# Performance work log

Measured on AMD Instinct MI355X. Metric: run time of the kernel, lower is better.

Reference implementation:

```python
import jax, jax.numpy as jnp
import numpy as np

IN_CH = 4096
OUT_CH = 4096
DENSITY = 0.1
BATCH = 8192


def setup_inputs() -> dict:
    key = jax.random.key(0)
    k_mask, k_w, k_b, k_x = jax.random.split(key, 4)
    # Fixed sparsity pattern, as in the torch module's sparse_mask.nonzero()
    mask = jax.random.bernoulli(k_mask, DENSITY, (OUT_CH, IN_CH))
    rows, cols = jnp.nonzero(mask)  # unique (row, col) pairs
    rows = rows.astype(jnp.int32)
    cols = cols.astype(jnp.int32)
    nnz = rows.shape[0]
    # Kaiming-style init per output row (approximate: uniform bound from mean fan-in)
    fan_in = jnp.maximum(jnp.sum(mask, axis=1).astype(jnp.float32), 1.0)  # [OUT_CH]
    gain = np.sqrt(2.0 / (1.0 + 5.0))  # leaky_relu gain with a=sqrt(5)
    std = gain / jnp.sqrt(fan_in)
    w_bound = np.sqrt(3.0) * std  # per-row bound
    u = jax.random.uniform(k_w, (nnz,), minval=-1.0, maxval=1.0)
    sparse_weight = u * w_bound[rows]
    b_bound = 1.0 / jnp.sqrt(fan_in)
    bias = jax.random.uniform(k_b, (OUT_CH,), minval=-1.0, maxval=1.0) * b_bound
    x = jax.random.normal(k_x, (BATCH, IN_CH), dtype=jnp.float32)
    return {
        "x": x,
        "sparse_weight": sparse_weight.astype(jnp.float32),
        "rows": rows,
        "cols": cols,
        "bias": bias.astype(jnp.float32),
    }


def reference(x, sparse_weight, rows, cols, bias):
    # Rebuild the (fixed-pattern) sparse weight as a dense [OUT_CH, IN_CH] matrix
    # (indices are unique, so .set matches the COO semantics), then y = x @ W^T + b.
    W = jnp.zeros((OUT_CH, IN_CH), dtype=sparse_weight.dtype).at[rows, cols].set(sparse_weight)
    return x @ W.T + bias  # [BATCH, OUT_CH]
```

## Files before the change

kernel.cpp:

```cpp
#include <hip/hip_runtime.h>
#include <hip/hip_bf16.h>

#define M_DIM 8192
#define N_DIM 4096
#define K_DIM 4096
#define BM 128
#define BN 128
#define BK 64

typedef __bf16 bf16x8 __attribute__((ext_vector_type(8)));
typedef float  f32x4  __attribute__((ext_vector_type(4)));
typedef unsigned short u16x8 __attribute__((ext_vector_type(8)));

#define ASYNC16(g, l)                                                          \
  __builtin_amdgcn_global_load_lds(                                            \
      (__attribute__((address_space(1))) void*)(g),                            \
      (__attribute__((address_space(3))) void*)(l), 16, 0, 0)

static __device__ __forceinline__ unsigned short f2bf(float f) {
  unsigned int u = __float_as_uint(f);
  u += 0x7fffu + ((u >> 16) & 1u);
  return (unsigned short)(u >> 16);
}

__global__ void sl_bounds(const int* __restrict__ rows, int* __restrict__ row_start,
                          int* __restrict__ row_end, int nnz) {
  int k = blockIdx.x * 256 + threadIdx.x;
  if (k >= nnz) return;
  int r = rows[k];
  if (k == 0 || rows[k - 1] != r) row_start[r] = k;
  if (k == nnz - 1 || rows[k + 1] != r) row_end[r] = k + 1;
}

__global__ __launch_bounds__(256) void sl_prep(
    const float4* __restrict__ x4, u16x8* __restrict__ xb,
    const float* __restrict__ vals, const int* __restrict__ cols,
    const int* __restrict__ row_start, const int* __restrict__ row_end,
    unsigned short* __restrict__ W) {
  const int b = blockIdx.x;
  if (b < N_DIM) {
    __shared__ __align__(16) unsigned short rowbuf[K_DIM];
    u16x8* rb8 = (u16x8*)rowbuf;
    u16x8 z = {};
    rb8[threadIdx.x] = z;
    rb8[256 + threadIdx.x] = z;
    __syncthreads();
    const int s = row_start[b];
    const int e = row_end[b];
    for (int k = s + threadIdx.x; k < e; k += 256)
      rowbuf[cols[k]] = f2bf(vals[k]);
    __syncthreads();
    u16x8* dst = (u16x8*)(W + (size_t)b * K_DIM);
    dst[threadIdx.x] = rb8[threadIdx.x];
    dst[256 + threadIdx.x] = rb8[256 + threadIdx.x];
  } else {
    const int i = (b - N_DIM) * 256 + threadIdx.x;
    float4 a = x4[2 * i];
    float4 c = x4[2 * i + 1];
    u16x8 o;
    o[0] = f2bf(a.x); o[1] = f2bf(a.y); o[2] = f2bf(a.z); o[3] = f2bf(a.w);
    o[4] = f2bf(c.x); o[5] = f2bf(c.y); o[6] = f2bf(c.z); o[7] = f2bf(c.w);
    xb[i] = o;
  }
}

__global__ __launch_bounds__(256) void sl_prep_bs(
    const float4* __restrict__ x4, u16x8* __restrict__ xb,
    const float* __restrict__ vals, const int* __restrict__ rows,
    const int* __restrict__ cols, unsigned short* __restrict__ W, int nnz) {
  const int b = blockIdx.x;
  if (b < N_DIM) {
    __shared__ __align__(16) unsigned short rowbuf[K_DIM];
    u16x8* rb8 = (u16x8*)rowbuf;
    u16x8 z = {};
    rb8[threadIdx.x] = z;
    rb8[256 + threadIdx.x] = z;
    __syncthreads();
    int l = 0, h = nnz;
    while (l < h) { int m = (l + h) >> 1; if (rows[m] < b) l = m + 1; else h = m; }
    const int s = l;
    h = nnz;
    while (l < h) { int m = (l + h) >> 1; if (rows[m] <= b) l = m + 1; else h = m; }
    const int e = l;
    for (int k = s + threadIdx.x; k < e; k += 256)
      rowbuf[cols[k]] = f2bf(vals[k]);
    __syncthreads();
    u16x8* dst = (u16x8*)(W + (size_t)b * K_DIM);
    dst[threadIdx.x] = rb8[threadIdx.x];
    dst[256 + threadIdx.x] = rb8[256 + threadIdx.x];
  } else {
    const int i = (b - N_DIM) * 256 + threadIdx.x;
    float4 a = x4[2 * i];
    float4 c = x4[2 * i + 1];
    u16x8 o;
    o[0] = f2bf(a.x); o[1] = f2bf(a.y); o[2] = f2bf(a.z); o[3] = f2bf(a.w);
    o[4] = f2bf(c.x); o[5] = f2bf(c.y); o[6] = f2bf(c.z); o[7] = f2bf(c.w);
    xb[i] = o;
  }
}

__global__ __launch_bounds__(256, 3) void sl_gemm_bias(
    const unsigned short* __restrict__ A,
    const unsigned short* __restrict__ B,
    const float* __restrict__ bias,
    float* __restrict__ C) {
  __shared__ __align__(16) unsigned short As[BM * BK];
  __shared__ __align__(16) unsigned short Bs[BN * BK];

  const int tid  = threadIdx.x;
  const int wave = tid >> 6;
  const int lane = tid & 63;
  const int m0 = blockIdx.x * BM;
  const int n0 = blockIdx.y * BN;

  const int srow = tid >> 3;
  const int scol = ((tid & 7) ^ ((tid >> 3) & 7)) * 8;
  const unsigned short* gA = A + (size_t)(m0 + srow) * K_DIM + scol;
  const unsigned short* gB = B + (size_t)(n0 + srow) * K_DIM + scol;
  unsigned short* lA = As + (size_t)(wave * 64) * 8;
  unsigned short* lB = Bs + (size_t)(wave * 64) * 8;
  const size_t GROW = (size_t)32 * K_DIM;
  const size_t LROW = (size_t)256 * 8;

  const int wm   = (wave >> 1) * 64;
  const int wn   = (wave & 1) * 64;
  const int fm   = lane & 15;
  const int quad = lane >> 4;
  const int sw   = fm & 7;

  f32x4 acc[4][4] = {};

#pragma unroll
  for (int r = 0; r < 4; ++r) {
    ASYNC16(gA + r * GROW, lA + r * LROW);
    ASYNC16(gB + r * GROW, lB + r * LROW);
  }
  gA += BK; gB += BK;

  for (int k0 = 0; k0 < K_DIM; k0 += BK) {
    __syncthreads();

    bf16x8 af[4][2], bfr[4][2];
#pragma unroll
    for (int t = 0; t < 4; ++t) {
#pragma unroll
      for (int h = 0; h < 2; ++h) {
        const int pA = ((h * 4 + quad) ^ sw) * 8;
        af[t][h]  = *(const bf16x8*)(As + (size_t)(wm + t * 16 + fm) * BK + pA);
        bfr[t][h] = *(const bf16x8*)(Bs + (size_t)(wn + t * 16 + fm) * BK + pA);
      }
    }
    __syncthreads();

    if (k0 + BK < K_DIM) {
#pragma unroll
      for (int r = 0; r < 4; ++r) {
        ASYNC16(gA + r * GROW, lA + r * LROW);
        ASYNC16(gB + r * GROW, lB + r * LROW);
      }
      gA += BK; gB += BK;
    }

#pragma unroll
    for (int h = 0; h < 2; ++h)
#pragma unroll
      for (int tm = 0; tm < 4; ++tm)
#pragma unroll
        for (int tn = 0; tn < 4; ++tn)
          acc[tm][tn] = __builtin_amdgcn_mfma_f32_16x16x32_bf16(
              af[tm][h], bfr[tn][h], acc[tm][tn], 0, 0, 0);
  }

  float bv[4];
#pragma unroll
  for (int tn = 0; tn < 4; ++tn) bv[tn] = bias[n0 + wn + tn * 16 + fm];

#pragma unroll
  for (int tm = 0; tm < 4; ++tm) {
    const int mbase = m0 + wm + tm * 16 + quad * 4;
#pragma unroll
    for (int tn = 0; tn < 4; ++tn) {
      const int n = n0 + wn + tn * 16 + fm;
      float* p = C + (size_t)mbase * N_DIM + n;
#pragma unroll
      for (int r = 0; r < 4; ++r)
        __builtin_nontemporal_store(acc[tm][tn][r] + bv[tn], p + (size_t)r * N_DIM);
    }
  }
}

__global__ void sl_naive(const float* __restrict__ x, const float* __restrict__ vals,
                         const int* __restrict__ rows, const int* __restrict__ cols,
                         const float* __restrict__ bias, float* __restrict__ out,
                         int nnz) {
  const int o = blockIdx.x;
  int l = 0, h = nnz;
  while (l < h) { int m = (l + h) >> 1; if (rows[m] < o) l = m + 1; else h = m; }
  const int s = l;
  h = nnz;
  while (l < h) { int m = (l + h) >> 1; if (rows[m] <= o) l = m + 1; else h = m; }
  const int e = l;
  const float bv = bias[o];
  for (int b = threadIdx.x; b < M_DIM; b += blockDim.x) {
    float acc = bv;
    const float* xb = x + (size_t)b * K_DIM;
    for (int k = s; k < e; ++k) acc += vals[k] * xb[cols[k]];
    out[(size_t)b * N_DIM + o] = acc;
  }
}

extern "C" void kernel_launch(void* const* d_in, const int* in_sizes, int n_in,
                              void* d_out, int out_size, void* d_ws, size_t ws_size,
                              hipStream_t stream) {
  const float* x    = (const float*)d_in[0];
  const float* vals = (const float*)d_in[1];
  const int*   rows = (const int*)d_in[2];
  const int*   cols = (const int*)d_in[3];
  const float* bias = (const float*)d_in[4];
  float* out = (float*)d_out;
  const int nnz = in_sizes[1];

  const size_t xb_bytes  = (size_t)M_DIM * K_DIM * 2;
  const size_t w_bytes   = (size_t)N_DIM * K_DIM * 2;
  const size_t idx_bytes = (size_t)2 * N_DIM * 4;

  const int cvt_blocks = (M_DIM * K_DIM) / 8 / 256;

  if (ws_size >= xb_bytes + w_bytes + idx_bytes) {
    unsigned short* xb = (unsigned short*)d_ws;
    unsigned short* W  = (unsigned short*)((char*)d_ws + xb_bytes);
    int* row_start = (int*)((char*)d_ws + xb_bytes + w_bytes);
    int* row_end   = row_start + N_DIM;

    hipMemsetAsync(row_start, 0, idx_bytes, stream);
    sl_bounds<<<(nnz + 255) / 256, 256, 0, stream>>>(rows, row_start, row_end, nnz);
    sl_prep<<<N_DIM + cvt_blocks, 256, 0, stream>>>(
        (const float4*)x, (u16x8*)xb, vals, cols, row_start, row_end, W);
    sl_gemm_bias<<<dim3(M_DIM / BM, N_DIM / BN), 256, 0, stream>>>(xb, W, bias, out);
  } else if (ws_size >= xb_bytes + w_bytes) {
    unsigned short* xb = (unsigned short*)d_ws;
    unsigned short* W  = (unsigned short*)((char*)d_ws + xb_bytes);
    sl_prep_bs<<<N_DIM + cvt_blocks, 256, 0, stream>>>(
        (const float4*)x, (u16x8*)xb, vals, rows, cols, W, nnz);
    sl_gemm_bias<<<dim3(M_DIM / BM, N_DIM / BN), 256, 0, stream>>>(xb, W, bias, out);
  } else {
    sl_naive<<<N_DIM, 256, 0, stream>>>(x, vals, rows, cols, bias, out, nnz);
  }
}
```

Measured before the change: 456.0 us.

## Fuse fp32-to-bf16 conversion of x into GEMM loads and swizzle block order

Drops the separate pass that converted x to bf16 in workspace. The GEMM now loads fp32 x tiles through registers, converts them with packed bf16 instructions and writes them to LDS, interleaved with the MFMA work on the previous tile. The bounds and memset path is removed in favour of binary-search weight prep, and block indices are remapped to improve L2 reuse. The trade-off is that the A operand no longer uses async global-to-LDS loads, and each GEMM block reads x as fp32, re-converting it once per N-tile.

Measured after the change: 971.8 us. +113.1%, slower.

```diff
diff --git a/kernel.cpp b/kernel.cpp
--- a/kernel.cpp
+++ b/kernel.cpp
@@ -23,84 +23,43 @@
   return (unsigned short)(u >> 16);
 }
 
-__global__ void sl_bounds(const int* __restrict__ rows, int* __restrict__ row_start,
-                          int* __restrict__ row_end, int nnz) {
-  int k = blockIdx.x * 256 + threadIdx.x;
-  if (k >= nnz) return;
-  int r = rows[k];
-  if (k == 0 || rows[k - 1] != r) row_start[r] = k;
-  if (k == nnz - 1 || rows[k + 1] != r) row_end[r] = k + 1;
-}
-
-__global__ __launch_bounds__(256) void sl_prep(
-    const float4* __restrict__ x4, u16x8* __restrict__ xb,
-    const float* __restrict__ vals, const int* __restrict__ cols,
-    const int* __restrict__ row_start, const int* __restrict__ row_end,
-    unsigned short* __restrict__ W) {
-  const int b = blockIdx.x;
-  if (b < N_DIM) {
-    __shared__ __align__(16) unsigned short rowbuf[K_DIM];
-    u16x8* rb8 = (u16x8*)rowbuf;
-    u16x8 z = {};
-    rb8[threadIdx.x] = z;
-    rb8[256 + threadIdx.x] = z;
-    __syncthreads();
-    const int s = row_start[b];
-    const int e = row_end[b];
-    for (int k = s + threadIdx.x; k < e; k += 256)
-      rowbuf[cols[k]] = f2bf(vals[k]);
-    __syncthreads();
-    u16x8* dst = (u16x8*)(W + (size_t)b * K_DIM);
-    dst[threadIdx.x] = rb8[threadIdx.x];
-    dst[256 + threadIdx.x] = rb8[256 + threadIdx.x];
-  } else {
-    const int i = (b - N_DIM) * 256 + threadIdx.x;
-    float4 a = x4[2 * i];
-    float4 c = x4[2 * i + 1];
-    u16x8 o;
-    o[0] = f2bf(a.x); o[1] = f2bf(a.y); o[2] = f2bf(a.z); o[3] = f2bf(a.w);
-    o[4] = f2bf(c.x); o[5] = f2bf(c.y); o[6] = f2bf(c.z); o[7] = f2bf(c.w);
-    xb[i] = o;
-  }
-}
-
-__global__ __launch_bounds__(256) void sl_prep_bs(
-    const float4* __restrict__ x4, u16x8* __restrict__ xb,
+static __device__ __forceinline__ void cvt8_store(unsigned short* dst,
+                                                  float4 a, float4 b) {
+  unsigned int p0, p1, p2, p3;
+  asm("v_cvt_pk_bf16_f32 %0, %1, %2" : "=v"(p0) : "v"(a.x), "v"(a.y));
+  asm("v_cvt_pk_bf16_f32 %0, %1, %2" : "=v"(p1) : "v"(a.z), "v"(a.w));
+  asm("v_cvt_pk_bf16_f32 %0, %1, %2" : "=v"(p2) : "v"(b.x), "v"(b.y));
+  asm("v_cvt_pk_bf16_f32 %0, %1, %2" : "=v"(p3) : "v"(b.z), "v"(b.w));
+  uint4 v; v.x = p0; v.y = p1; v.z = p2; v.w = p3;
+  *(uint4*)dst = v;
+}
+
+__global__ __launch_bounds__(256) void sl_prep_w(
     const float* __restrict__ vals, const int* __restrict__ rows,
     const int* __restrict__ cols, unsigned short* __restrict__ W, int nnz) {
   const int b = blockIdx.x;
-  if (b < N_DIM) {
-    __shared__ __align__(16) unsigned short rowbuf[K_DIM];
-    u16x8* rb8 = (u16x8*)rowbuf;
-    u16x8 z = {};
-    rb8[threadIdx.x] = z;
-    rb8[256 + threadIdx.x] = z;
-    __syncthreads();
-    int l = 0, h = nnz;
-    while (l < h) { int m = (l + h) >> 1; if (rows[m] < b) l = m + 1; else h = m; }
-    const int s = l;
-    h = nnz;
-    while (l < h) { int m = (l + h) >> 1; if (rows[m] <= b) l = m + 1; else h = m; }
-    const int e = l;
-    for (int k = s + threadIdx.x; k < e; k += 256)
-      rowbuf[cols[k]] = f2bf(vals[k]);
-    __syncthreads();
-    u16x8* dst = (u16x8*)(W + (size_t)b * K_DIM);
-    dst[threadIdx.x] = rb8[threadIdx.x];
-    dst[256 + threadIdx.x] = rb8[256 + threadIdx.x];
-  } else {
-    const int i = (b - N_DIM) * 256 + threadIdx.x;
-    float4 a = x4[2 * i];
-    float4 c = x4[2 * i + 1];
-    u16x8 o;
-    o[0] = f2bf(a.x); o[1] = f2bf(a.y); o[2] = f2bf(a.z); o[3] = f2bf(a.w);
-    o[4] = f2bf(c.x); o[5] = f2bf(c.y); o[6] = f2bf(c.z); o[7] = f2bf(c.w);
-    xb[i] = o;
-  }
+  __shared__ __align__(16) unsigned short rowbuf[K_DIM];
+  u16x8* rb8 = (u16x8*)rowbuf;
+  u16x8 z = {};
+  rb8[threadIdx.x] = z;
+  rb8[256 + threadIdx.x] = z;
+  __syncthreads();
+  int l = 0, h = nnz;
+  while (l < h) { int m = (l + h) >> 1; if (rows[m] < b) l = m + 1; else h = m; }
+  const int s = l;
+  h = nnz;
+  while (l < h) { int m = (l + h) >> 1; if (rows[m] <= b) l = m + 1; else h = m; }
+  const int e = l;
+  for (int k = s + threadIdx.x; k < e; k += 256)
+    rowbuf[cols[k]] = f2bf(vals[k]);
+  __syncthreads();
+  u16x8* dst = (u16x8*)(W + (size_t)b * K_DIM);
+  dst[threadIdx.x] = rb8[threadIdx.x];
+  dst[256 + threadIdx.x] = rb8[256 + threadIdx.x];
 }
 
 __global__ __launch_bounds__(256, 3) void sl_gemm_bias(
-    const unsigned short* __restrict__ A,
+    const float* __restrict__ A,
     const unsigned short* __restrict__ B,
     const float* __restrict__ bias,
     float* __restrict__ C) {
@@ -110,17 +69,23 @@
   const int tid  = threadIdx.x;
   const int wave = tid >> 6;
   const int lane = tid & 63;
-  const int m0 = blockIdx.x * BM;
-  const int n0 = blockIdx.y * BN;
+
+  const int orig = blockIdx.y * (M_DIM / BM) + blockIdx.x;
+  const int swz  = (orig & 7) * ((M_DIM / BM) * (N_DIM / BN) / 8) + (orig >> 3);
+  const int nt   = swz & (N_DIM / BN - 1);
+  const int mt   = swz >> 5;
+  const int m0 = mt * BM;
+  const int n0 = nt * BN;
 
   const int srow = tid >> 3;
-  const int scol = ((tid & 7) ^ ((tid >> 3) & 7)) * 8;
-  const unsigned short* gA = A + (size_t)(m0 + srow) * K_DIM + scol;
-  const unsigned short* gB = B + (size_t)(n0 + srow) * K_DIM + scol;
-  unsigned short* lA = As + (size_t)(wave * 64) * 8;
+  const int pc   = (tid & 7) ^ (srow & 7);
+  const float* gA = A + (size_t)(m0 + srow) * K_DIM + (tid & 7) * 8;
+  const unsigned short* gB = B + (size_t)(n0 + srow) * K_DIM + pc * 8;
+  unsigned short* wA = As + (size_t)srow * BK + pc * 8;
   unsigned short* lB = Bs + (size_t)(wave * 64) * 8;
   const size_t GROW = (size_t)32 * K_DIM;
   const size_t LROW = (size_t)256 * 8;
+  const size_t WROW = (size_t)32 * BK;
 
   const int wm   = (wave >> 1) * 64;
   const int wn   = (wave & 1) * 64;
@@ -131,11 +96,23 @@
   f32x4 acc[4][4] = {};
 
 #pragma unroll
-  for (int r = 0; r < 4; ++r) {
-    ASYNC16(gA + r * GROW, lA + r * LROW);
-    ASYNC16(gB + r * GROW, lB + r * LROW);
-  }
-  gA += BK; gB += BK;
+  for (int r = 0; r < 4; ++r) ASYNC16(gB + r * GROW, lB + r * LROW);
+  {
+    float4 a0 = *(const float4*)(gA);
+    float4 a1 = *(const float4*)(gA + 4);
+    float4 a2 = *(const float4*)(gA + GROW);
+    float4 a3 = *(const float4*)(gA + GROW + 4);
+    cvt8_store(wA, a0, a1);
+    cvt8_store(wA + WROW, a2, a3);
+    float4 a4 = *(const float4*)(gA + 2 * GROW);
+    float4 a5 = *(const float4*)(gA + 2 * GROW + 4);
+    float4 a6 = *(const float4*)(gA + 3 * GROW);
+    float4 a7 = *(const float4*)(gA + 3 * GROW + 4);
+    cvt8_store(wA + 2 * WROW, a4, a5);
+    cvt8_store(wA + 3 * WROW, a6, a7);
+  }
+  gA += BK;
+  gB += BK;
 
   for (int k0 = 0; k0 < K_DIM; k0 += BK) {
     __syncthreads();
@@ -144,31 +121,58 @@
 #pragma unroll
     for (int t = 0; t < 4; ++t) {
 #pragma unroll
-      for (int h = 0; h < 2; ++h) {
-        const int pA = ((h * 4 + quad) ^ sw) * 8;
-        af[t][h]  = *(const bf16x8*)(As + (size_t)(wm + t * 16 + fm) * BK + pA);
-        bfr[t][h] = *(const bf16x8*)(Bs + (size_t)(wn + t * 16 + fm) * BK + pA);
+      for (int hh = 0; hh < 2; ++hh) {
+        const int p = ((hh * 4 + quad) ^ sw) * 8;
+        af[t][hh]  = *(const bf16x8*)(As + (size_t)(wm + t * 16 + fm) * BK + p);
+        bfr[t][hh] = *(const bf16x8*)(Bs + (size_t)(wn + t * 16 + fm) * BK + p);
       }
     }
+
+    const bool more = (k0 + BK < K_DIM);
+    float4 a0, a1, a2, a3;
+    if (more) {
+      a0 = *(const float4*)(gA);
+      a1 = *(const float4*)(gA + 4);
+      a2 = *(const float4*)(gA + GROW);
+      a3 = *(const float4*)(gA + GROW + 4);
+    }
     __syncthreads();
 
-    if (k0 + BK < K_DIM) {
-#pragma unroll
-      for (int r = 0; r < 4; ++r) {
-        ASYNC16(gA + r * GROW, lA + r * LROW);
-        ASYNC16(gB + r * GROW, lB + r * LROW);
-      }
-      gA += BK; gB += BK;
-    }
-
-#pragma unroll
-    for (int h = 0; h < 2; ++h)
-#pragma unroll
-      for (int tm = 0; tm < 4; ++tm)
-#pragma unroll
-        for (int tn = 0; tn < 4; ++tn)
-          acc[tm][tn] = __builtin_amdgcn_mfma_f32_16x16x32_bf16(
-              af[tm][h], bfr[tn][h], acc[tm][tn], 0, 0, 0);
+    if (more) {
+#pragma unroll
+      for (int r = 0; r < 4; ++r) ASYNC16(gB + r * GROW, lB + r * LROW);
+      gB += BK;
+    }
+
+#pragma unroll
+    for (int tm = 0; tm < 4; ++tm)
+#pragma unroll
+      for (int tn = 0; tn < 4; ++tn)
+        acc[tm][tn] = __builtin_amdgcn_mfma_f32_16x16x32_bf16(
+            af[tm][0], bfr[tn][0], acc[tm][tn], 0, 0, 0);
+
+    float4 a4, a5, a6, a7;
+    if (more) {
+      cvt8_store(wA, a0, a1);
+      cvt8_store(wA + WROW, a2, a3);
+      a4 = *(const float4*)(gA + 2 * GROW);
+      a5 = *(const float4*)(gA + 2 * GROW + 4);
+      a6 = *(const float4*)(gA + 3 * GROW);
+      a7 = *(const float4*)(gA + 3 * GROW + 4);
+    }
+
+#pragma unroll
+    for (int tm = 0; tm < 4; ++tm)
+#pragma unroll
+      for (int tn = 0; tn < 4; ++tn)
+        acc[tm][tn] = __builtin_amdgcn_mfma_f32_16x16x32_bf16(
+            af[tm][1], bfr[tn][1], acc[tm][tn], 0, 0, 0);
+
+    if (more) {
+      cvt8_store(wA + 2 * WROW, a4, a5);
+      cvt8_store(wA + 3 * WROW, a6, a7);
+      gA += BK;
+    }
   }
 
   float bv[4];
@@ -220,29 +224,12 @@
   float* out = (float*)d_out;
   const int nnz = in_sizes[1];
 
-  const size_t xb_bytes  = (size_t)M_DIM * K_DIM * 2;
-  const size_t w_bytes   = (size_t)N_DIM * K_DIM * 2;
-  const size_t idx_bytes = (size_t)2 * N_DIM * 4;
-
-  const int cvt_blocks = (M_DIM * K_DIM) / 8 / 256;
-
-  if (ws_size >= xb_bytes + w_bytes + idx_bytes) {
-    unsigned short* xb = (unsigned short*)d_ws;
-    unsigned short* W  = (unsigned short*)((char*)d_ws + xb_bytes);
-    int* row_start = (int*)((char*)d_ws + xb_bytes + w_bytes);
-    int* row_end   = row_start + N_DIM;
-
-    hipMemsetAsync(row_start, 0, idx_bytes, stream);
-    sl_bounds<<<(nnz + 255) / 256, 256, 0, stream>>>(rows, row_start, row_end, nnz);
-    sl_prep<<<N_DIM + cvt_blocks, 256, 0, stream>>>(
-        (const float4*)x, (u16x8*)xb, vals, cols, row_start, row_end, W);
-    sl_gemm_bias<<<dim3(M_DIM / BM, N_DIM / BN), 256, 0, stream>>>(xb, W, bias, out);
-  } else if (ws_size >= xb_bytes + w_bytes) {
-    unsigned short* xb = (unsigned short*)d_ws;
-    unsigned short* W  = (unsigned short*)((char*)d_ws + xb_bytes);
-    sl_prep_bs<<<N_DIM + cvt_blocks, 256, 0, stream>>>(
-        (const float4*)x, (u16x8*)xb, vals, rows, cols, W, nnz);
-    sl_gemm_bias<<<dim3(M_DIM / BM, N_DIM / BN), 256, 0, stream>>>(xb, W, bias, out);
+  const size_t w_bytes = (size_t)N_DIM * K_DIM * 2;
+
+  if (ws_size >= w_bytes) {
+    unsigned short* W = (unsigned short*)d_ws;
+    sl_prep_w<<<N_DIM, 256, 0, stream>>>(vals, rows, cols, W, nnz);
+    sl_gemm_bias<<<dim3(M_DIM / BM, N_DIM / BN), 256, 0, stream>>>(x, W, bias, out);
   } else {
     sl_naive<<<N_DIM, 256, 0, stream>>>(x, vals, rows, cols, bias, out, nnz);
   }
```

## Restructure GEMM to 256x128 tiles with 3-stage LDS pipeline and tile swizzle

Applied to the files above, without the earlier changes.

The bf16 GEMM moves to 512-thread blocks with 256x128 output tiles, a triple-buffered LDS ring filled by async global-to-LDS loads, and explicit waitcnt and barrier phases that interleave loads with MFMA bursts under raised wave priority. Block indices are remapped so neighbouring blocks share A/B tiles in L2. The preprocessing drops the bounds kernel and memset and always uses the binary-search prep kernel. The goal is to hide memory latency and cut launch overhead, at the cost of fewer resident blocks, about 144KB of dynamic LDS per block, and more hand-tuned sync.

After: 549.6 us. 20.5% more time.

```diff
diff --git a/kernel.cpp b/kernel.cpp
--- a/kernel.cpp
+++ b/kernel.cpp
@@ -4,9 +4,13 @@
 #define M_DIM 8192
 #define N_DIM 4096
 #define K_DIM 4096
-#define BM 128
+#define BM 256
 #define BN 128
 #define BK 64
+#define A_ELEMS (BM * BK)
+#define B_ELEMS (BN * BK)
+#define LDS_BYTES ((3 * (A_ELEMS + B_ELEMS)) * 2)
+#define NT_TILES (K_DIM / BK)
 
 typedef __bf16 bf16x8 __attribute__((ext_vector_type(8)));
 typedef float  f32x4  __attribute__((ext_vector_type(4)));
@@ -21,47 +25,6 @@
   unsigned int u = __float_as_uint(f);
   u += 0x7fffu + ((u >> 16) & 1u);
   return (unsigned short)(u >> 16);
-}
-
-__global__ void sl_bounds(const int* __restrict__ rows, int* __restrict__ row_start,
-                          int* __restrict__ row_end, int nnz) {
-  int k = blockIdx.x * 256 + threadIdx.x;
-  if (k >= nnz) return;
-  int r = rows[k];
-  if (k == 0 || rows[k - 1] != r) row_start[r] = k;
-  if (k == nnz - 1 || rows[k + 1] != r) row_end[r] = k + 1;
-}
-
-__global__ __launch_bounds__(256) void sl_prep(
-    const float4* __restrict__ x4, u16x8* __restrict__ xb,
-    const float* __restrict__ vals, const int* __restrict__ cols,
-    const int* __restrict__ row_start, const int* __restrict__ row_end,
-    unsigned short* __restrict__ W) {
-  const int b = blockIdx.x;
-  if (b < N_DIM) {
-    __shared__ __align__(16) unsigned short rowbuf[K_DIM];
-    u16x8* rb8 = (u16x8*)rowbuf;
-    u16x8 z = {};
-    rb8[threadIdx.x] = z;
-    rb8[256 + threadIdx.x] = z;
-    __syncthreads();
-    const int s = row_start[b];
-    const int e = row_end[b];
-    for (int k = s + threadIdx.x; k < e; k += 256)
-      rowbuf[cols[k]] = f2bf(vals[k]);
-    __syncthreads();
-    u16x8* dst = (u16x8*)(W + (size_t)b * K_DIM);
-    dst[threadIdx.x] = rb8[threadIdx.x];
-    dst[256 + threadIdx.x] = rb8[256 + threadIdx.x];
-  } else {
-    const int i = (b - N_DIM) * 256 + threadIdx.x;
-    float4 a = x4[2 * i];
-    float4 c = x4[2 * i + 1];
-    u16x8 o;
-    o[0] = f2bf(a.x); o[1] = f2bf(a.y); o[2] = f2bf(a.z); o[3] = f2bf(a.w);
-    o[4] = f2bf(c.x); o[5] = f2bf(c.y); o[6] = f2bf(c.z); o[7] = f2bf(c.w);
-    xb[i] = o;
-  }
 }
 
 __global__ __launch_bounds__(256) void sl_prep_bs(
@@ -99,87 +62,128 @@
   }
 }
 
-__global__ __launch_bounds__(256, 3) void sl_gemm_bias(
+__global__ __launch_bounds__(512, 2) void sl_gemm_bias(
     const unsigned short* __restrict__ A,
     const unsigned short* __restrict__ B,
     const float* __restrict__ bias,
     float* __restrict__ C) {
-  __shared__ __align__(16) unsigned short As[BM * BK];
-  __shared__ __align__(16) unsigned short Bs[BN * BK];
+  extern __shared__ __align__(16) unsigned short lds[];
+  unsigned short* As = lds;
+  unsigned short* Bs = lds + 3 * A_ELEMS;
 
   const int tid  = threadIdx.x;
   const int wave = tid >> 6;
   const int lane = tid & 63;
-  const int m0 = blockIdx.x * BM;
-  const int n0 = blockIdx.y * BN;
+
+  const int orig = blockIdx.y * (M_DIM / BM) + blockIdx.x;
+  const int swz  = (orig & 7) * 128 + (orig >> 3);
+  const int mt   = swz >> 5;
+  const int nt   = swz & 31;
+  const int m0 = mt * BM;
+  const int n0 = nt * BN;
 
   const int srow = tid >> 3;
-  const int scol = ((tid & 7) ^ ((tid >> 3) & 7)) * 8;
+  const int scol = ((tid & 7) ^ (srow & 7)) * 8;
   const unsigned short* gA = A + (size_t)(m0 + srow) * K_DIM + scol;
   const unsigned short* gB = B + (size_t)(n0 + srow) * K_DIM + scol;
-  unsigned short* lA = As + (size_t)(wave * 64) * 8;
-  unsigned short* lB = Bs + (size_t)(wave * 64) * 8;
-  const size_t GROW = (size_t)32 * K_DIM;
-  const size_t LROW = (size_t)256 * 8;
-
-  const int wm   = (wave >> 1) * 64;
-  const int wn   = (wave & 1) * 64;
+  const size_t GROW = (size_t)64 * K_DIM;
+  const int ldsw = wave * 64 * 8;
+
+  const int wm   = (wave >> 2) * 128;
+  const int wn   = (wave & 3) * 32;
   const int fm   = lane & 15;
   const int quad = lane >> 4;
-  const int sw   = fm & 7;
-
-  f32x4 acc[4][4] = {};
-
-#pragma unroll
-  for (int r = 0; r < 4; ++r) {
-    ASYNC16(gA + r * GROW, lA + r * LROW);
-    ASYNC16(gB + r * GROW, lB + r * LROW);
-  }
-  gA += BK; gB += BK;
-
-  for (int k0 = 0; k0 < K_DIM; k0 += BK) {
-    __syncthreads();
-
-    bf16x8 af[4][2], bfr[4][2];
-#pragma unroll
-    for (int t = 0; t < 4; ++t) {
-#pragma unroll
-      for (int h = 0; h < 2; ++h) {
-        const int pA = ((h * 4 + quad) ^ sw) * 8;
-        af[t][h]  = *(const bf16x8*)(As + (size_t)(wm + t * 16 + fm) * BK + pA);
-        bfr[t][h] = *(const bf16x8*)(Bs + (size_t)(wn + t * 16 + fm) * BK + pA);
-      }
-    }
-    __syncthreads();
-
-    if (k0 + BK < K_DIM) {
-#pragma unroll
-      for (int r = 0; r < 4; ++r) {
-        ASYNC16(gA + r * GROW, lA + r * LROW);
-        ASYNC16(gB + r * GROW, lB + r * LROW);
-      }
-      gA += BK; gB += BK;
-    }
-
-#pragma unroll
-    for (int h = 0; h < 2; ++h)
-#pragma unroll
-      for (int tm = 0; tm < 4; ++tm)
-#pragma unroll
-        for (int tn = 0; tn < 4; ++tn)
-          acc[tm][tn] = __builtin_amdgcn_mfma_f32_16x16x32_bf16(
-              af[tm][h], bfr[tn][h], acc[tm][tn], 0, 0, 0);
-  }
-
-  float bv[4];
-#pragma unroll
-  for (int tn = 0; tn < 4; ++tn) bv[tn] = bias[n0 + wn + tn * 16 + fm];
-
-#pragma unroll
-  for (int tm = 0; tm < 4; ++tm) {
+  int offA[8], offB[2], pk[2];
+#pragma unroll
+  for (int i = 0; i < 8; ++i) offA[i] = (wm + i * 16 + fm) * BK;
+#pragma unroll
+  for (int i = 0; i < 2; ++i) offB[i] = (wn + i * 16 + fm) * BK;
+#pragma unroll
+  for (int i = 0; i < 2; ++i) pk[i] = ((i * 4 + quad) ^ (fm & 7)) * 8;
+
+  f32x4 acc[8][2] = {};
+
+#pragma unroll
+  for (int tt = 0; tt < 2; ++tt) {
+#pragma unroll
+    for (int r = 0; r < 4; ++r)
+      ASYNC16(gA + tt * BK + r * GROW, As + tt * A_ELEMS + ldsw + r * 4096);
+#pragma unroll
+    for (int r = 0; r < 2; ++r)
+      ASYNC16(gB + tt * BK + r * GROW, Bs + tt * B_ELEMS + ldsw + r * 4096);
+  }
+  gA += 2 * BK;
+  gB += 2 * BK;
+  asm volatile("s_waitcnt vmcnt(6)" ::: "memory");
+  __builtin_amdgcn_sched_barrier(0);
+  __builtin_amdgcn_s_barrier();
+
+#define PHASE(MS, KK, STAGE_CODE, TAIL_CODE)                                   \
+  {                                                                            \
+    bf16x8 a0 = *(const bf16x8*)(Ac + offA[(MS)*4 + 0] + pk[KK]);              \
+    bf16x8 a1 = *(const bf16x8*)(Ac + offA[(MS)*4 + 1] + pk[KK]);              \
+    bf16x8 a2 = *(const bf16x8*)(Ac + offA[(MS)*4 + 2] + pk[KK]);              \
+    bf16x8 a3 = *(const bf16x8*)(Ac + offA[(MS)*4 + 3] + pk[KK]);              \
+    bf16x8 b0 = *(const bf16x8*)(Bc + offB[0] + pk[KK]);                       \
+    bf16x8 b1 = *(const bf16x8*)(Bc + offB[1] + pk[KK]);                       \
+    STAGE_CODE                                                                 \
+    __builtin_amdgcn_s_barrier();                                              \
+    asm volatile("s_waitcnt lgkmcnt(0)" ::: "memory");                         \
+    __builtin_amdgcn_sched_barrier(0);                                         \
+    __builtin_amdgcn_s_setprio(1);                                             \
+    acc[(MS)*4+0][0] = __builtin_amdgcn_mfma_f32_16x16x32_bf16(a0, b0, acc[(MS)*4+0][0], 0, 0, 0); \
+    acc[(MS)*4+0][1] = __builtin_amdgcn_mfma_f32_16x16x32_bf16(a0, b1, acc[(MS)*4+0][1], 0, 0, 0); \
+    acc[(MS)*4+1][0] = __builtin_amdgcn_mfma_f32_16x16x32_bf16(a1, b0, acc[(MS)*4+1][0], 0, 0, 0); \
+    acc[(MS)*4+1][1] = __builtin_amdgcn_mfma_f32_16x16x32_bf16(a1, b1, acc[(MS)*4+1][1], 0, 0, 0); \
+    acc[(MS)*4+2][0] = __builtin_amdgcn_mfma_f32_16x16x32_bf16(a2, b0, acc[(MS)*4+2][0], 0, 0, 0); \
+    acc[(MS)*4+2][1] = __builtin_amdgcn_mfma_f32_16x16x32_bf16(a2, b1, acc[(MS)*4+2][1], 0, 0, 0); \
+    acc[(MS)*4+3][0] = __builtin_amdgcn_mfma_f32_16x16x32_bf16(a3, b0, acc[(MS)*4+3][0], 0, 0, 0); \
+    acc[(MS)*4+3][1] = __builtin_amdgcn_mfma_f32_16x16x32_bf16(a3, b1, acc[(MS)*4+3][1], 0, 0, 0); \
+    __builtin_amdgcn_s_setprio(0);                                             \
+    TAIL_CODE                                                                  \
+    __builtin_amdgcn_s_barrier();                                              \
+  }
+
+  int cur = 0, nxt = 2;
+  for (int t = 0; t < NT_TILES; ++t) {
+    const unsigned short* Ac = As + cur * A_ELEMS;
+    const unsigned short* Bc = Bs + cur * B_ELEMS;
+    unsigned short* Asn = As + nxt * A_ELEMS + ldsw;
+    unsigned short* Bsn = Bs + nxt * B_ELEMS + ldsw;
+    const bool more = (t < NT_TILES - 2);
+
+    PHASE(0, 0,
+          if (more) { ASYNC16(gA, Asn); ASYNC16(gA + GROW, Asn + 4096); }, )
+    PHASE(0, 1,
+          if (more) { ASYNC16(gA + 2 * GROW, Asn + 2 * 4096);
+                      ASYNC16(gA + 3 * GROW, Asn + 3 * 4096); }, )
+    PHASE(1, 0,
+          if (more) { ASYNC16(gB, Bsn); }, )
+    PHASE(1, 1,
+          if (more) { ASYNC16(gB + GROW, Bsn + 4096); },
+          if (more) {
+            asm volatile("s_waitcnt vmcnt(6)" ::: "memory");
+            __builtin_amdgcn_sched_barrier(0);
+          } else if (t == NT_TILES - 2) {
+            asm volatile("s_waitcnt vmcnt(0)" ::: "memory");
+            __builtin_amdgcn_sched_barrier(0);
+          } )
+
+    if (more) { gA += BK; gB += BK; }
+    cur = (cur == 2) ? 0 : cur + 1;
+    nxt = (nxt == 2) ? 0 : nxt + 1;
+  }
+#undef PHASE
+
+  float bv[2];
+#pragma unroll
+  for (int tn = 0; tn < 2; ++tn) bv[tn] = bias[n0 + wn + tn * 16 + fm];
+
+#pragma unroll
+  for (int tm = 0; tm < 8; ++tm) {
     const int mbase = m0 + wm + tm * 16 + quad * 4;
 #pragma unroll
-    for (int tn = 0; tn < 4; ++tn) {
+    for (int tn = 0; tn < 2; ++tn) {
       const int n = n0 + wn + tn * 16 + fm;
       float* p = C + (size_t)mbase * N_DIM + n;
 #pragma unroll
@@ -220,29 +224,26 @@
   float* out = (float*)d_out;
   const int nnz = in_sizes[1];
 
-  const size_t xb_bytes  = (size_t)M_DIM * K_DIM * 2;
-  const size_t w_bytes   = (size_t)N_DIM * K_DIM * 2;
-  const size_t idx_bytes = (size_t)2 * N_DIM * 4;
-
-  const int cvt_blocks = (M_DIM * K_DIM) / 8 / 256;
-
-  if (ws_size >= xb_bytes + w_bytes + idx_bytes) {
+  const size_t xb_bytes = (size_t)M_DIM * K_DIM * 2;
+  const size_t w_bytes  = (size_t)N_DIM * K_DIM * 2;
+  const int cvt_blocks  = (M_DIM * K_DIM) / 8 / 256;
+
+  if (ws_size >= xb_bytes + w_bytes) {
     unsigned short* xb = (unsigned short*)d_ws;
     unsigned short* W  = (unsigned short*)((char*)d_ws + xb_bytes);
-    int* row_start = (int*)((char*)d_ws + xb_bytes + w_bytes);
-    int* row_end   = row_start + N_DIM;
-
-    hipMemsetAsync(row_start, 0, idx_bytes, stream);
-    sl_bounds<<<(nnz + 255) / 256, 256, 0, stream>>>(rows, row_start, row_end, nnz);
-    sl_prep<<<N_DIM + cvt_blocks, 256, 0, stream>>>(
-        (const float4*)x, (u16x8*)xb, vals, cols, row_start, row_end, W);
-    sl_gemm_bias<<<dim3(M_DIM / BM, N_DIM / BN), 256, 0, stream>>>(xb, W, bias, out);
-  } else if (ws_size >= xb_bytes + w_bytes) {
-    unsigned short* xb = (unsigned short*)d_ws;
-    unsigned short* W  = (unsigned short*)((char*)d_ws + xb_bytes);
+
+    static bool attr_done = false;
+    if (!attr_done) {
+      (void)hipFuncSetAttribute((const void*)sl_gemm_bias,
+                                hipFuncAttributeMaxDynamicSharedMemorySize,
+                                LDS_BYTES);
+      attr_done = true;
+    }
+
     sl_prep_bs<<<N_DIM + cvt_blocks, 256, 0, stream>>>(
         (const float4*)x, (u16x8*)xb, vals, rows, cols, W, nnz);
-    sl_gemm_bias<<<dim3(M_DIM / BM, N_DIM / BN), 256, 0, stream>>>(xb, W, bias, out);
+    sl_gemm_bias<<<dim3(M_DIM / BM, N_DIM / BN), 512, LDS_BYTES, stream>>>(
+        xb, W, bias, out);
   } else {
     sl_naive<<<N_DIM, 256, 0, stream>>>(x, vals, rows, cols, bias, out, nnz);
   }
```
